# Optimization experiments

Measured on AMD Instinct MI355X. Metric: run time of the kernel, lower is better.

The kernel has to match this reference:

```python
import jax, jax.numpy as jnp
import numpy as np

GROUP_SIZE = 64  # quantization group size along in_features (K)


def setup_inputs() -> dict:
    key = jax.random.key(0)
    k1, k2, k3, k4, k5 = jax.random.split(key, 5)
    M, K, N = 32, 8192, 8192
    num_groups = K // GROUP_SIZE
    x = jax.random.normal(k1, (M, K), dtype=jnp.float32)
    # packed int4 weights: two nibbles per byte along K -> [N, K//2]
    packed_weight = jax.random.randint(k2, (N, K // 2), 0, 256, dtype=jnp.int32)
    scales = jax.random.uniform(k3, (N, num_groups), dtype=jnp.float32) * 0.02 + 1e-3
    zeros = jax.random.uniform(k4, (N, num_groups), dtype=jnp.float32) * 15.0
    bias_param = jax.random.normal(k5, (N,), dtype=jnp.float32)
    return {"x": x, "packed_weight": packed_weight, "scales": scales,
            "zeros": zeros, "bias_param": bias_param}


def reference(x, packed_weight, scales, zeros, bias_param):
    # x: [M, K] float; packed_weight: [N, K//2] int (uint8 semantics)
    # scales/zeros: [N, num_groups]; bias_param: [N]
    K = x.shape[-1]
    k = jnp.arange(K)
    shift = (k % 2) * 4                     # low nibble for even k, high for odd
    # unpack int4: q[n, k] in [0, 15]
    q = (packed_weight[:, k // 2] >> shift[None, :]) & 15   # [N, K]
    gidx = k // GROUP_SIZE                                  # [K]
    # group-wise dequant: (q - zero) * scale
    w = (q.astype(jnp.float32) - zeros[:, gidx]) * scales[:, gidx]  # [N, K]
    out = jnp.einsum('mk,nk->mn', x, w) + bias_param[None, :]        # [M, N]
    return out
```

## Files before the change

### kernel.cpp

```cpp
#include <hip/hip_runtime.h>
#include <hip/hip_bf16.h>
#include <stdint.h>


#define KK 8192
#define NN 8192
#define KP 4096
#define NG 128
#define BN 128
#define KSPLIT 8
#define KSPW 8
#define NKS 256

typedef __attribute__((ext_vector_type(8))) short short8;
typedef __attribute__((ext_vector_type(4))) float floatx4;
typedef __attribute__((ext_vector_type(4))) int int4v;

__device__ __forceinline__ unsigned pack_bf16x2(float lo, float hi) {
    union { __hip_bfloat162 h; unsigned u; } c;
    c.h = __float22bfloat162_rn(make_float2(lo, hi));
    return c.u;
}

__device__ __forceinline__ unsigned dq2(int q, float sc, float zs) {
    float lo = fmaf((float)(q & 15),        sc, zs);
    float hi = fmaf((float)((q >> 4) & 15), sc, zs);
    unsigned ua = __float_as_uint(lo); ua += 0x7fffu + ((ua >> 16) & 1u);
    unsigned ub = __float_as_uint(hi); ub += 0x7fffu + ((ub >> 16) & 1u);
    return __builtin_amdgcn_perm(ub, ua, 0x07060302);
}

__global__ void prep_kernel(const float* __restrict__ x, const float* __restrict__ bias,
                            ushort* __restrict__ xb, float* __restrict__ out,
                            int xconv_blocks)
{
    const int bx = blockIdx.x;
    if (bx < xconv_blocks) {
        const int tid = bx * 256 + threadIdx.x;
        const int l   = tid & 63;
        const int ks  = (tid >> 6) & 255;
        const int mt  = tid >> 14;
        const int m   = (l & 15) + 16 * mt;
        const int kb  = ks * 32 + (l >> 4) * 8;
        const float* src = x + (size_t)m * KK + kb;
        const float4 a = *(const float4*)(src);
        const float4 b = *(const float4*)(src + 4);
        *(uint4*)(xb + (size_t)tid * 8) =
            make_uint4(pack_bf16x2(a.x, a.y), pack_bf16x2(a.z, a.w),
                       pack_bf16x2(b.x, b.y), pack_bf16x2(b.z, b.w));
    } else {
        const int f4 = (bx - xconv_blocks) * 256 + threadIdx.x;
        const int n4 = f4 & (NN / 4 - 1);
        ((float4*)out)[f4] = ((const float4*)bias)[n4];
    }
}

__global__ __launch_bounds__(256, 2)
void gptq_mfma_main(const int*   __restrict__ pw,
                    const float* __restrict__ scales,
                    const float* __restrict__ zeros,
                    const ushort* __restrict__ xb,
                    float* __restrict__ out)
{
    __shared__ __align__(16) float smem[4 * 32 * 132];
    float (*sc_lds)[132] = (float (*)[132])smem;
    float (*zs_lds)[132] = (float (*)[132])(smem + 16 * 132);
    float (*red)[32][132] = (float (*)[32][132])smem;

    const int tid  = threadIdx.x;
    const int lane = tid & 63;
    const int wave = tid >> 6;
    const int kh   = blockIdx.x & (KSPLIT - 1);
    const int n0   = (blockIdx.x >> 3) * BN;
    const int nl   = lane & 15;
    const int kq   = lane >> 4;
    const int ks0  = kh * 32 + wave * KSPW;

    {
        const int r  = tid >> 1;
        const int go = (tid & 1) * 8;
        const float* sp = scales + (size_t)(n0 + r) * NG + kh * 16 + go;
        const float* zp = zeros  + (size_t)(n0 + r) * NG + kh * 16 + go;
#pragma unroll
        for (int t = 0; t < 2; ++t) {
            const float4 s4 = *(const float4*)(sp + t * 4);
            const float4 z4 = *(const float4*)(zp + t * 4);
            sc_lds[go + t*4 + 0][r] = s4.x; zs_lds[go + t*4 + 0][r] = -z4.x * s4.x;
            sc_lds[go + t*4 + 1][r] = s4.y; zs_lds[go + t*4 + 1][r] = -z4.y * s4.y;
            sc_lds[go + t*4 + 2][r] = s4.z; zs_lds[go + t*4 + 2][r] = -z4.z * s4.z;
            sc_lds[go + t*4 + 3][r] = s4.w; zs_lds[go + t*4 + 3][r] = -z4.w * s4.w;
        }
    }
    __syncthreads();

    const int* pwp[8];
#pragma unroll
    for (int f = 0; f < 8; ++f)
        pwp[f] = pw + (size_t)(n0 + f * 16 + nl) * KP + kq * 4;
    const uint4* xfp = (const uint4*)xb;

    floatx4 acc[8][2];
#pragma unroll
    for (int f = 0; f < 8; ++f)
#pragma unroll
        for (int mt = 0; mt < 2; ++mt)
            acc[f][mt] = (floatx4){0.f, 0.f, 0.f, 0.f};

    int4v pb[2][8];
    uint4 xa[2][2];

    {
        const int ks = ks0;
#pragma unroll
        for (int f = 0; f < 8; ++f)
            pb[0][f] = *(const int4v*)(pwp[f] + ks * 16);
        xa[0][0] = xfp[(size_t)(0 * NKS + ks) * 64 + lane];
        xa[0][1] = xfp[(size_t)(1 * NKS + ks) * 64 + lane];
    }

#pragma unroll
    for (int i = 0; i < KSPW; ++i) {
        const int slot = i & 1;
        if (i + 1 < KSPW) {
            const int ks = ks0 + i + 1;
            const int ps = slot ^ 1;
#pragma unroll
            for (int f = 0; f < 8; ++f)
                pb[ps][f] = *(const int4v*)(pwp[f] + ks * 16);
            xa[ps][0] = xfp[(size_t)(0 * NKS + ks) * 64 + lane];
            xa[ps][1] = xfp[(size_t)(1 * NKS + ks) * 64 + lane];
        }
        const int gl = (wave * KSPW + i) >> 1;

        union { uint4 v; short8 sv; } a0, a1;
        a0.v = xa[slot][0];
        a1.v = xa[slot][1];
#pragma unroll
        for (int f = 0; f < 8; ++f) {
            const float sc = sc_lds[gl][f * 16 + nl];
            const float zs = zs_lds[gl][f * 16 + nl];
            union { uint4 v; short8 sv; } bf;
            const int4v p = pb[slot][f];
            bf.v.x = dq2(p.x, sc, zs);
            bf.v.y = dq2(p.y, sc, zs);
            bf.v.z = dq2(p.z, sc, zs);
            bf.v.w = dq2(p.w, sc, zs);
            acc[f][0] = __builtin_amdgcn_mfma_f32_16x16x32_bf16(a0.sv, bf.sv, acc[f][0], 0, 0, 0);
            acc[f][1] = __builtin_amdgcn_mfma_f32_16x16x32_bf16(a1.sv, bf.sv, acc[f][1], 0, 0, 0);
        }
    }

    __syncthreads();

#pragma unroll
    for (int f = 0; f < 8; ++f)
#pragma unroll
        for (int mt = 0; mt < 2; ++mt)
#pragma unroll
            for (int r = 0; r < 4; ++r)
                red[wave][mt * 16 + kq * 4 + r][f * 16 + nl] = acc[f][mt][r];
    __syncthreads();

#pragma unroll
    for (int j = 0; j < 16; ++j) {
        const int e = j * 256 + tid;
        const int m = e >> 7, c = e & 127;
        const float s = red[0][m][c] + red[1][m][c] + red[2][m][c] + red[3][m][c];
        atomicAdd(out + (size_t)m * NN + n0 + c, s);
    }
}

__global__ __launch_bounds__(256, 4)
void gptq_mfma_fallback(const int*   __restrict__ pw,
                        const float* __restrict__ scales,
                        const float* __restrict__ zeros,
                        const float* __restrict__ x,
                        float* __restrict__ out)
{
    __shared__ float s_lds[64][17];
    __shared__ float z_lds[64][17];
    __shared__ float red[4][2][256];

    const int tid  = threadIdx.x;
    const int lane = tid & 63;
    const int wave = tid >> 6;
    const int kh   = blockIdx.x & 1;
    const int n0   = (blockIdx.x >> 1) * 16;
    const int g0   = kh * 64;

    {
        const int r  = tid >> 4;
        const int gb = (tid & 15) * 4;
        const float4 s4 = *(const float4*)(scales + (size_t)(n0 + r) * NG + g0 + gb);
        const float4 z4 = *(const float4*)(zeros  + (size_t)(n0 + r) * NG + g0 + gb);
        s_lds[gb + 0][r] = s4.x; s_lds[gb + 1][r] = s4.y;
        s_lds[gb + 2][r] = s4.z; s_lds[gb + 3][r] = s4.w;
        z_lds[gb + 0][r] = z4.x; z_lds[gb + 1][r] = z4.y;
        z_lds[gb + 2][r] = z4.z; z_lds[gb + 3][r] = z4.w;
    }
    __syncthreads();

    const int nl = lane & 15;
    const int kq = lane >> 4;
    const int* pwp = pw + (size_t)(n0 + nl) * KP + kq * 4;
    const int ks0 = kh * 128 + wave * 32;

    auto load_xfrag = [&](int mt, int ks) -> uint4 {
        const float* src = x + (size_t)(nl + 16 * mt) * KK + ks * 32 + kq * 8;
        const float4 a = *(const float4*)(src);
        const float4 b = *(const float4*)(src + 4);
        return make_uint4(pack_bf16x2(a.x, a.y), pack_bf16x2(a.z, a.w),
                          pack_bf16x2(b.x, b.y), pack_bf16x2(b.z, b.w));
    };

    floatx4 acc0 = {0.f, 0.f, 0.f, 0.f};
    floatx4 acc1 = {0.f, 0.f, 0.f, 0.f};
    int4v pwb[4];
    uint4 x0b[4], x1b[4];

#pragma unroll
    for (int i = 0; i < 3; ++i) {
        const int ks = ks0 + i;
        pwb[i] = *(const int4v*)(pwp + ks * 16);
        x0b[i] = load_xfrag(0, ks);
        x1b[i] = load_xfrag(1, ks);
    }

#pragma unroll 4
    for (int i = 0; i < 32; ++i) {
        const int slot = i & 3;
        if (i + 3 < 32) {
            const int ks = ks0 + i + 3;
            const int ps = (i + 3) & 3;
            pwb[ps] = *(const int4v*)(pwp + ks * 16);
            x0b[ps] = load_xfrag(0, ks);
            x1b[ps] = load_xfrag(1, ks);
        }
        const int gl  = (wave * 32 + i) >> 1;
        const float sc = s_lds[gl][nl];
        const float zs = -z_lds[gl][nl] * sc;

        union { uint4 v; short8 sv; } bf, a0, a1;
        const int4v p = pwb[slot];
        bf.v.x = dq2(p.x, sc, zs);
        bf.v.y = dq2(p.y, sc, zs);
        bf.v.z = dq2(p.z, sc, zs);
        bf.v.w = dq2(p.w, sc, zs);
        a0.v = x0b[slot];
        a1.v = x1b[slot];
        acc0 = __builtin_amdgcn_mfma_f32_16x16x32_bf16(a0.sv, bf.sv, acc0, 0, 0, 0);
        acc1 = __builtin_amdgcn_mfma_f32_16x16x32_bf16(a1.sv, bf.sv, acc1, 0, 0, 0);
    }

#pragma unroll
    for (int r = 0; r < 4; ++r) {
        const int row = kq * 4 + r;
        red[wave][0][row * 16 + nl] = acc0[r];
        red[wave][1][row * 16 + nl] = acc1[r];
    }
    __syncthreads();

#pragma unroll
    for (int i = 0; i < 2; ++i) {
        const int e   = i * 256 + tid;
        const int mt  = e >> 8;
        const int idx = e & 255;
        const float s = red[0][mt][idx] + red[1][mt][idx] + red[2][mt][idx] + red[3][mt][idx];
        atomicAdd(out + (size_t)(mt * 16 + (idx >> 4)) * NN + n0 + (idx & 15), s);
    }
}

extern "C" void kernel_launch(void* const* d_in, const int* in_sizes, int n_in,
                              void* d_out, int out_size, void* d_ws, size_t ws_size,
                              hipStream_t stream) {
    const float* x      = (const float*)d_in[0];
    const int*   pw     = (const int*)  d_in[1];
    const float* scales = (const float*)d_in[2];
    const float* zeros  = (const float*)d_in[3];
    const float* bias   = (const float*)d_in[4];
    float* out = (float*)d_out;

    const size_t need = (size_t)32768 * 16;
    if (d_ws != nullptr && ws_size >= need) {
        ushort* xb = (ushort*)d_ws;
        prep_kernel<<<128 + 256, 256, 0, stream>>>(x, bias, xb, out, 128);
        gptq_mfma_main<<<(NN / BN) * KSPLIT, 256, 0, stream>>>(pw, scales, zeros, xb, out);
    } else {
        prep_kernel<<<256, 256, 0, stream>>>(x, bias, nullptr, out, 0);
        gptq_mfma_fallback<<<1024, 256, 0, stream>>>(pw, scales, zeros, x, out);
    }
}
```

Baseline: 210.9 us.

## Stage packed weights through LDS with direct global-to-LDS loads and XOR swizzle

Packed int4 weights now go straight from global memory into a double-buffered, XOR-swizzled LDS tile using global_load_lds, replacing the per-lane register prefetch. Each wave loads a contiguous row slice, so global reads become fully coalesced 256-byte rows instead of strided 16-byte per-row reads. Waves interleave across k-steps round by round, with a block barrier each round. LDS use grows to 80 KB, which may limit occupancy to one block per CU, and the barriers add synchronisation.

```diff
diff --git a/kernel.cpp b/kernel.cpp
--- a/kernel.cpp
+++ b/kernel.cpp
@@ -9,8 +9,8 @@
 #define NG 128
 #define BN 128
 #define KSPLIT 8
-#define KSPW 8
 #define NKS 256
+#define ROUNDS 8
 
 typedef __attribute__((ext_vector_type(8))) short short8;
 typedef __attribute__((ext_vector_type(4))) float floatx4;
@@ -28,6 +28,12 @@
     unsigned ua = __float_as_uint(lo); ua += 0x7fffu + ((ua >> 16) & 1u);
     unsigned ub = __float_as_uint(hi); ub += 0x7fffu + ((ub >> 16) & 1u);
     return __builtin_amdgcn_perm(ub, ua, 0x07060302);
+}
+
+__device__ __forceinline__ void gload_lds16(const void* g, void* l) {
+    __builtin_amdgcn_global_load_lds(
+        (const __attribute__((address_space(1))) unsigned int*)g,
+        (__attribute__((address_space(3))) unsigned int*)l, 16, 0, 0);
 }
 
 __global__ void prep_kernel(const float* __restrict__ x, const float* __restrict__ bias,
@@ -62,9 +68,9 @@
                     const ushort* __restrict__ xb,
                     float* __restrict__ out)
 {
-    __shared__ __align__(16) float smem[4 * 32 * 132];
-    float (*sc_lds)[132] = (float (*)[132])smem;
-    float (*zs_lds)[132] = (float (*)[132])(smem + 16 * 132);
+    __shared__ __align__(16) unsigned char smem[81920];
+    float* sc_lds = (float*)(smem + 65536);
+    float* zs_lds = (float*)(smem + 73728);
     float (*red)[32][132] = (float (*)[32][132])smem;
 
     const int tid  = threadIdx.x;
@@ -74,30 +80,47 @@
     const int n0   = (blockIdx.x >> 3) * BN;
     const int nl   = lane & 15;
     const int kq   = lane >> 4;
-    const int ks0  = kh * 32 + wave * KSPW;
-
-    {
-        const int r  = tid >> 1;
+
+    {
+        const int rr = tid >> 1;
         const int go = (tid & 1) * 8;
-        const float* sp = scales + (size_t)(n0 + r) * NG + kh * 16 + go;
-        const float* zp = zeros  + (size_t)(n0 + r) * NG + kh * 16 + go;
+        const float* sp = scales + (size_t)(n0 + rr) * NG + kh * 16 + go;
+        const float* zp = zeros  + (size_t)(n0 + rr) * NG + kh * 16 + go;
 #pragma unroll
         for (int t = 0; t < 2; ++t) {
             const float4 s4 = *(const float4*)(sp + t * 4);
             const float4 z4 = *(const float4*)(zp + t * 4);
-            sc_lds[go + t*4 + 0][r] = s4.x; zs_lds[go + t*4 + 0][r] = -z4.x * s4.x;
-            sc_lds[go + t*4 + 1][r] = s4.y; zs_lds[go + t*4 + 1][r] = -z4.y * s4.y;
-            sc_lds[go + t*4 + 2][r] = s4.z; zs_lds[go + t*4 + 2][r] = -z4.z * s4.z;
-            sc_lds[go + t*4 + 3][r] = s4.w; zs_lds[go + t*4 + 3][r] = -z4.w * s4.w;
-        }
-    }
-    __syncthreads();
-
-    const int* pwp[8];
-#pragma unroll
-    for (int f = 0; f < 8; ++f)
-        pwp[f] = pw + (size_t)(n0 + f * 16 + nl) * KP + kq * 4;
+            sc_lds[(go + t*4 + 0)*128 + rr] = s4.x; zs_lds[(go + t*4 + 0)*128 + rr] = -z4.x * s4.x;
+            sc_lds[(go + t*4 + 1)*128 + rr] = s4.y; zs_lds[(go + t*4 + 1)*128 + rr] = -z4.y * s4.y;
+            sc_lds[(go + t*4 + 2)*128 + rr] = s4.z; zs_lds[(go + t*4 + 2)*128 + rr] = -z4.z * s4.z;
+            sc_lds[(go + t*4 + 3)*128 + rr] = s4.w; zs_lds[(go + t*4 + 3)*128 + rr] = -z4.w * s4.w;
+        }
+    }
+
+    const unsigned char* gsrc[8];
+    {
+        const unsigned char* pwB = (const unsigned char*)pw + (size_t)kh * 2048;
+#pragma unroll
+        for (int i = 0; i < 8; ++i) {
+            const int rl = 32 * wave + 4 * i + kq;
+            const int o  = (nl * 16) ^ ((rl & 7) << 4);
+            gsrc[i] = pwB + (size_t)(n0 + rl) * 16384 + o;
+        }
+    }
+
+    {
+        unsigned char* dst = smem + wave * 8192;
+#pragma unroll
+        for (int i = 0; i < 8; ++i)
+            gload_lds16(gsrc[i], dst + i * 1024);
+    }
     const uint4* xfp = (const uint4*)xb;
+    uint4 xa[2][2];
+    {
+        const int ks = kh * 32 + wave;
+        xa[0][0] = xfp[(size_t)(0 * NKS + ks) * 64 + lane];
+        xa[0][1] = xfp[(size_t)(1 * NKS + ks) * 64 + lane];
+    }
 
     floatx4 acc[8][2];
 #pragma unroll
@@ -106,41 +129,33 @@
         for (int mt = 0; mt < 2; ++mt)
             acc[f][mt] = (floatx4){0.f, 0.f, 0.f, 0.f};
 
-    int4v pb[2][8];
-    uint4 xa[2][2];
-
-    {
-        const int ks = ks0;
-#pragma unroll
-        for (int f = 0; f < 8; ++f)
-            pb[0][f] = *(const int4v*)(pwp[f] + ks * 16);
-        xa[0][0] = xfp[(size_t)(0 * NKS + ks) * 64 + lane];
-        xa[0][1] = xfp[(size_t)(1 * NKS + ks) * 64 + lane];
-    }
-
-#pragma unroll
-    for (int i = 0; i < KSPW; ++i) {
-        const int slot = i & 1;
-        if (i + 1 < KSPW) {
-            const int ks = ks0 + i + 1;
-            const int ps = slot ^ 1;
-#pragma unroll
-            for (int f = 0; f < 8; ++f)
-                pb[ps][f] = *(const int4v*)(pwp[f] + ks * 16);
-            xa[ps][0] = xfp[(size_t)(0 * NKS + ks) * 64 + lane];
-            xa[ps][1] = xfp[(size_t)(1 * NKS + ks) * 64 + lane];
-        }
-        const int gl = (wave * KSPW + i) >> 1;
+    __syncthreads();
+
+#pragma unroll
+    for (int r = 0; r < ROUNDS; ++r) {
+        if (r + 1 < ROUNDS) {
+            unsigned char* dst = smem + ((r + 1) & 1) * 32768 + wave * 8192;
+#pragma unroll
+            for (int i = 0; i < 8; ++i)
+                gload_lds16(gsrc[i] + (size_t)(r + 1) * 256, dst + i * 1024);
+            const int ksn = kh * 32 + (r + 1) * 4 + wave;
+            xa[(r + 1) & 1][0] = xfp[(size_t)(0 * NKS + ksn) * 64 + lane];
+            xa[(r + 1) & 1][1] = xfp[(size_t)(1 * NKS + ksn) * 64 + lane];
+        }
+
+        const int gl = (r * 4 + wave) >> 1;
+        const unsigned char* pwb = smem + (r & 1) * 32768;
+        const int boff = nl * 256 + ((wave * 64 + kq * 16) ^ ((nl & 7) << 4));
 
         union { uint4 v; short8 sv; } a0, a1;
-        a0.v = xa[slot][0];
-        a1.v = xa[slot][1];
+        a0.v = xa[r & 1][0];
+        a1.v = xa[r & 1][1];
 #pragma unroll
         for (int f = 0; f < 8; ++f) {
-            const float sc = sc_lds[gl][f * 16 + nl];
-            const float zs = zs_lds[gl][f * 16 + nl];
+            const float sc = sc_lds[gl * 128 + f * 16 + nl];
+            const float zs = zs_lds[gl * 128 + f * 16 + nl];
+            const int4v p = *(const int4v*)(pwb + f * 4096 + boff);
             union { uint4 v; short8 sv; } bf;
-            const int4v p = pb[slot][f];
             bf.v.x = dq2(p.x, sc, zs);
             bf.v.y = dq2(p.y, sc, zs);
             bf.v.z = dq2(p.z, sc, zs);
@@ -148,17 +163,16 @@
             acc[f][0] = __builtin_amdgcn_mfma_f32_16x16x32_bf16(a0.sv, bf.sv, acc[f][0], 0, 0, 0);
             acc[f][1] = __builtin_amdgcn_mfma_f32_16x16x32_bf16(a1.sv, bf.sv, acc[f][1], 0, 0, 0);
         }
-    }
-
-    __syncthreads();
+        __syncthreads();
+    }
 
 #pragma unroll
     for (int f = 0; f < 8; ++f)
 #pragma unroll
         for (int mt = 0; mt < 2; ++mt)
 #pragma unroll
-            for (int r = 0; r < 4; ++r)
-                red[wave][mt * 16 + kq * 4 + r][f * 16 + nl] = acc[f][mt][r];
+            for (int rr = 0; rr < 4; ++rr)
+                red[wave][mt * 16 + kq * 4 + rr][f * 16 + nl] = acc[f][mt][rr];
     __syncthreads();
 
 #pragma unroll
```

New measurement: 207.8 us. About the same (-1.5%).
